# Performance work log

Hardware: AMD Instinct MI355X
Metric: run time of the kernel (lower is better)

Reference implementation:

```python
import jax, jax.numpy as jnp
import numpy as np

DIM = 192  # init dim; input channels = 2*DIM, output channels = DIM
EPS = 1e-5


def setup_inputs() -> dict:
    key = jax.random.key(0)
    k1, k2 = jax.random.split(key)
    x = jax.random.normal(k1, (2, 16, 32, 32, 2 * DIM), dtype=jnp.float32)
    W = jax.random.normal(k2, (2 * DIM, 8 * DIM), dtype=jnp.float32) * 0.02
    gamma = jnp.ones((2 * DIM,), dtype=jnp.float32)
    beta = jnp.zeros((2 * DIM,), dtype=jnp.float32)
    return {"x": x, "W": W, "gamma": gamma, "beta": beta}


def reference(x, W, gamma, beta):
    dim = DIM
    b, d, h, w, c = x.shape  # c == 2*dim
    # LayerNorm over last dim (biased variance, as torch)
    mu = jnp.mean(x, axis=-1, keepdims=True)
    var = jnp.var(x, axis=-1, keepdims=True)
    xn = (x - mu) * jax.lax.rsqrt(var + EPS) * gamma + beta
    # Linear expansion 2*dim -> 8*dim (no bias)
    xe = jnp.einsum('bdhwc,ce->bdhwe', xn, W)  # (b,d,h,w,8*dim)
    ch = lambda i: xe[..., i * dim:(i + 1) * dim]
    z = jnp.zeros((b, d, h, w, dim), dtype=xe.dtype)
    # Faithful to the torch code: parities (0,1,0) and (0,0,1) are written
    # are NEVER written (stay zero). Index = pd*4 + ph*2 + pw.
    grid = jnp.stack([
        ch(0), ch(6),  # (0,0,0), (0,0,1)
        ch(5), z,      # (0,1,0), (0,1,1)
        ch(1), ch(4),  # (1,0,0), (1,0,1)
        z,     ch(7),  # (1,1,0), (1,1,1)
    ], axis=4)  # (b,d,h,w,8,dim)
    grid = grid.reshape(b, d, h, w, 2, 2, 2, dim)
    # interleave parity axes: (b, d,pd, h,ph, w,pw, dim) -> (b,2d,2h,2w,dim)
    out = grid.transpose(0, 1, 4, 2, 5, 3, 6, 7).reshape(b, 2 * d, 2 * h, 2 * w, dim)
    return out
```

## Files before the change

### kernel.cpp

```cpp
#include <hip/hip_runtime.h>
#include <hip/hip_bf16.h>
#include <stdint.h>


typedef __attribute__((ext_vector_type(4))) float f32x4;
typedef __attribute__((ext_vector_type(8))) short s16x8;
typedef __attribute__((ext_vector_type(4))) unsigned short u16x4;
typedef const __attribute__((address_space(1))) void gvoid_t;
typedef __attribute__((address_space(3))) void lvoid_t;

__device__ __forceinline__ int ob_of_p(int p) {
    const int w = p & 31, h = (p >> 5) & 31, d = (p >> 10) & 15, b = p >> 14;
    return b * 25165824 + d * 1572864 + h * 24576 + w * 384;
}

__device__ __forceinline__ unsigned short f2bf(float f) {
    unsigned u = __builtin_bit_cast(unsigned, f);
    u += 0x7fffu + ((u >> 16) & 1u);
    return (unsigned short)(u >> 16);
}

__global__ __launch_bounds__(256) void ln_kernel(const float* __restrict__ x,
                                                 const float* __restrict__ gamma,
                                                 const float* __restrict__ beta,
                                                 float* __restrict__ outf) {
    const int wv = threadIdx.x >> 6;
    const int l  = threadIdx.x & 63;
    const int p  = blockIdx.x * 4 + wv;
    const float* row = x + (size_t)p * 384;
    f32x4 v0 = *(const f32x4*)(row + l * 4);
    f32x4 v1 = {0.f, 0.f, 0.f, 0.f};
    if (l < 32) v1 = *(const f32x4*)(row + 256 + l * 4);
    float s  = v0[0]+v0[1]+v0[2]+v0[3] + v1[0]+v1[1]+v1[2]+v1[3];
    float s2 = v0[0]*v0[0]+v0[1]*v0[1]+v0[2]*v0[2]+v0[3]*v0[3]
             + v1[0]*v1[0]+v1[1]*v1[1]+v1[2]*v1[2]+v1[3]*v1[3];
    #pragma unroll
    for (int off = 32; off >= 1; off >>= 1) {
        s  += __shfl_xor(s,  off);
        s2 += __shfl_xor(s2, off);
    }
    const float mu = s * (1.f / 384.f);
    const float rs = rsqrtf(s2 * (1.f / 384.f) - mu * mu + 1e-5f);
    unsigned short* dst = (unsigned short*)(outf + ob_of_p(p) + 12480);
    f32x4 g0 = *(const f32x4*)(gamma + l * 4);
    f32x4 b0 = *(const f32x4*)(beta  + l * 4);
    u16x4 o0;
    #pragma unroll
    for (int j = 0; j < 4; ++j) o0[j] = f2bf((v0[j] - mu) * rs * g0[j] + b0[j]);
    *(u16x4*)(dst + l * 4) = o0;
    if (l < 32) {
        f32x4 g1 = *(const f32x4*)(gamma + 256 + l * 4);
        f32x4 b1 = *(const f32x4*)(beta  + 256 + l * 4);
        u16x4 o1;
        #pragma unroll
        for (int j = 0; j < 4; ++j) o1[j] = f2bf((v1[j] - mu) * rs * g1[j] + b1[j]);
        *(u16x4*)(dst + 256 + l * 4) = o1;
    }
}

__global__ __launch_bounds__(256) void wt_kernel(const float* __restrict__ W,
                                                 float* __restrict__ outf) {
    const int t = blockIdx.x * 256 + threadIdx.x;
    const int k = t % 384;
    const int n = t / 384;
    const int s = n / 192;
    const int oc = (s < 2 ? s : s + 2) * 192 + (n % 192);
    const float v = W[(size_t)k * 1536 + oc];
    unsigned short* dst = (unsigned short*)(outf + ob_of_p(n) + 798720);
    dst[k] = f2bf(v);
}

__global__ __launch_bounds__(256) void gemm_kernel(float* __restrict__ outf) {
    __shared__ char lds[32768];
    const char* gbase = (const char*)outf;
    const int tid = threadIdx.x;
    const int wv = tid >> 6, l = tid & 63;
    int bid = blockIdx.x;
    bid = (bid & 7) * 288 + (bid >> 3);
    const int mt = bid / 9, nt = bid % 9;
    const int m0 = mt * 128, n0 = nt * 128;

    size_t srcA[4], srcB[4];
    int ldsA[4], ldsB[4];
    #pragma unroll
    for (int i = 0; i < 4; ++i) {
        const int r = wv * 32 + i * 8 + (l >> 3);
        const int swz = ((l & 7) * 16) ^ ((r & 7) << 4);
        srcA[i] = (size_t)(ob_of_p(m0 + r) + 12480)  * 4 + swz;
        srcB[i] = (size_t)(ob_of_p(n0 + r) + 798720) * 4 + swz;
        ldsA[i] = (wv * 32 + i * 8) * 128;
        ldsB[i] = 16384 + (wv * 32 + i * 8) * 128;
    }

    f32x4 acc[4][4];
    const f32x4 fz = {0.f, 0.f, 0.f, 0.f};
    #pragma unroll
    for (int m = 0; m < 4; ++m)
        #pragma unroll
        for (int n = 0; n < 4; ++n) acc[m][n] = fz;

    const int wm = wv >> 1, wn = wv & 1;
    int arow[4], brow[4];
    #pragma unroll
    for (int i = 0; i < 4; ++i) {
        arow[i] = wm * 64 + i * 16 + (l & 15);
        brow[i] = wn * 64 + i * 16 + (l & 15);
    }
    const int kbyte0 = (l >> 4) * 16;

    for (int t = 0; t < 6; ++t) {
        const int kb = t * 128;
        #pragma unroll
        for (int i = 0; i < 4; ++i)
            __builtin_amdgcn_global_load_lds((gvoid_t*)(gbase + srcA[i] + kb),
                                             (lvoid_t*)(lds + ldsA[i]), 16, 0, 0);
        #pragma unroll
        for (int i = 0; i < 4; ++i)
            __builtin_amdgcn_global_load_lds((gvoid_t*)(gbase + srcB[i] + kb),
                                             (lvoid_t*)(lds + ldsB[i]), 16, 0, 0);
        __syncthreads();
        #pragma unroll
        for (int kk = 0; kk < 2; ++kk) {
            const int kbyte = kbyte0 + kk * 64;
            s16x8 a[4], b[4];
            #pragma unroll
            for (int m = 0; m < 4; ++m)
                a[m] = *(const s16x8*)(lds + arow[m] * 128 + (kbyte ^ ((arow[m] & 7) << 4)));
            #pragma unroll
            for (int n = 0; n < 4; ++n)
                b[n] = *(const s16x8*)(lds + 16384 + brow[n] * 128 + (kbyte ^ ((brow[n] & 7) << 4)));
            #pragma unroll
            for (int m = 0; m < 4; ++m)
                #pragma unroll
                for (int n = 0; n < 4; ++n)
                    acc[m][n] = __builtin_amdgcn_mfma_f32_16x16x32_bf16(a[m], b[n], acc[m][n], 0, 0, 0);
        }
        __syncthreads();
    }

    int coladd[4];
    #pragma unroll
    for (int n = 0; n < 4; ++n) {
        const int gnb = n0 + wn * 64 + n * 16;
        const int s = gnb / 192;
        int d;
        if      (s == 0) d = 0;
        else if (s == 1) d = 786432;
        else if (s == 2) d = 786624;
        else if (s == 3) d = 12288;
        else if (s == 4) d = 192;
        else             d = 798912;
        coladd[n] = d + (gnb % 192) + (l & 15);
    }
    const int pb = m0 + wm * 64 + (l >> 4) * 4;
    #pragma unroll
    for (int m = 0; m < 4; ++m) {
        #pragma unroll
        for (int r = 0; r < 4; ++r) {
            const int p  = pb + m * 16 + r;
            const int ob = ob_of_p(p);
            #pragma unroll
            for (int n = 0; n < 4; ++n)
                outf[ob + coladd[n]] = acc[m][n][r];
        }
    }
}

__global__ __launch_bounds__(256) void zero_kernel(float* __restrict__ outf) {
    const int idx = blockIdx.x * 256 + threadIdx.x;
    const int f4 = idx % 48;
    const int pr = (idx / 48) & 1;
    const int p  = idx / 96;
    const f32x4 z = {0.f, 0.f, 0.f, 0.f};
    *(f32x4*)(outf + ob_of_p(p) + (pr ? 798720 : 12480) + f4 * 4) = z;
}

extern "C" void kernel_launch(void* const* d_in, const int* in_sizes, int n_in,
                              void* d_out, int out_size, void* d_ws, size_t ws_size,
                              hipStream_t stream) {
    const float* x     = (const float*)d_in[0];
    const float* W     = (const float*)d_in[1];
    const float* gamma = (const float*)d_in[2];
    const float* beta  = (const float*)d_in[3];
    float* out = (float*)d_out;
    ln_kernel  <<<8192,  256, 0, stream>>>(x, gamma, beta, out);
    wt_kernel  <<<1728,  256, 0, stream>>>(W, out);
    gemm_kernel<<<2304,  256, 0, stream>>>(out);
    zero_kernel<<<12288, 256, 0, stream>>>(out);
}
```

Measured before the change: 86.04 us.

## Stage operands in workspace, fuse zero fill into LN, double-buffer GEMM A tiles

When the workspace is large enough, the normalized activations and the reordered bf16 weights go to a contiguous workspace buffer instead of being scattered into the zero slots of the output. The zero-slot fill moves into the LayerNorm kernel, which removes the separate zero kernel launch. The GEMM reads B fragments straight from global memory into registers and double-buffers the A tile in LDS, overlapping the next tile's load with the MFMAs using explicit vmcnt waits. The cost is extra workspace memory and more fragile hand-written scheduling and waitcnt logic. The old path is kept as a fallback when the workspace is too small.

```diff
diff --git a/kernel.cpp b/kernel.cpp
--- a/kernel.cpp
+++ b/kernel.cpp
@@ -19,6 +19,169 @@
     u += 0x7fffu + ((u >> 16) & 1u);
     return (unsigned short)(u >> 16);
 }
+
+
+__global__ __launch_bounds__(256) void ln2_kernel(const float* __restrict__ x,
+                                                  const float* __restrict__ gamma,
+                                                  const float* __restrict__ beta,
+                                                  float* __restrict__ outf,
+                                                  unsigned short* __restrict__ xn) {
+    const int wv = threadIdx.x >> 6;
+    const int l  = threadIdx.x & 63;
+    const int p  = blockIdx.x * 4 + wv;
+    const float* row = x + (size_t)p * 384;
+    f32x4 v0 = *(const f32x4*)(row + l * 4);
+    f32x4 v1 = {0.f, 0.f, 0.f, 0.f};
+    if (l < 32) v1 = *(const f32x4*)(row + 256 + l * 4);
+    float s  = v0[0]+v0[1]+v0[2]+v0[3] + v1[0]+v1[1]+v1[2]+v1[3];
+    float s2 = v0[0]*v0[0]+v0[1]*v0[1]+v0[2]*v0[2]+v0[3]*v0[3]
+             + v1[0]*v1[0]+v1[1]*v1[1]+v1[2]*v1[2]+v1[3]*v1[3];
+    #pragma unroll
+    for (int off = 32; off >= 1; off >>= 1) {
+        s  += __shfl_xor(s,  off);
+        s2 += __shfl_xor(s2, off);
+    }
+    const float mu = s * (1.f / 384.f);
+    const float rs = rsqrtf(s2 * (1.f / 384.f) - mu * mu + 1e-5f);
+    unsigned short* dst = xn + (size_t)p * 384;
+    f32x4 g0 = *(const f32x4*)(gamma + l * 4);
+    f32x4 b0 = *(const f32x4*)(beta  + l * 4);
+    u16x4 o0;
+    #pragma unroll
+    for (int j = 0; j < 4; ++j) o0[j] = f2bf((v0[j] - mu) * rs * g0[j] + b0[j]);
+    *(u16x4*)(dst + l * 4) = o0;
+    if (l < 32) {
+        f32x4 g1 = *(const f32x4*)(gamma + 256 + l * 4);
+        f32x4 b1 = *(const f32x4*)(beta  + 256 + l * 4);
+        u16x4 o1;
+        #pragma unroll
+        for (int j = 0; j < 4; ++j) o1[j] = f2bf((v1[j] - mu) * rs * g1[j] + b1[j]);
+        *(u16x4*)(dst + 256 + l * 4) = o1;
+    }
+    if (l < 48) {
+        const int ob = ob_of_p(p);
+        const f32x4 z = {0.f, 0.f, 0.f, 0.f};
+        *(f32x4*)(outf + ob + 12480  + l * 4) = z;
+        *(f32x4*)(outf + ob + 798720 + l * 4) = z;
+    }
+}
+
+__global__ __launch_bounds__(256) void wt2_kernel(const float* __restrict__ W,
+                                                  unsigned short* __restrict__ wt) {
+    const int t = blockIdx.x * 256 + threadIdx.x;
+    const int k = t % 384;
+    const int n = t / 384;
+    const int s = n / 192;
+    const int oc = (s < 2 ? s : s + 2) * 192 + (n % 192);
+    wt[(size_t)n * 384 + k] = f2bf(W[(size_t)k * 1536 + oc]);
+}
+
+__global__ __launch_bounds__(256) void gemm2_kernel(const unsigned short* __restrict__ xn,
+                                                    const unsigned short* __restrict__ wt,
+                                                    float* __restrict__ outf) {
+    __shared__ char lds[32768];
+    const char* xb = (const char*)xn;
+    const char* wb = (const char*)wt;
+    const int tid = threadIdx.x;
+    const int wv = tid >> 6, l = tid & 63;
+    int bid = blockIdx.x;
+    bid = (bid & 7) * 288 + (bid >> 3);
+    const int mt = bid / 9, nt = bid % 9;
+    const int m0 = mt * 128, n0 = nt * 128;
+    const int wm = wv >> 1, wn = wv & 1;
+
+    size_t srcA[4]; int ldsA[4];
+    #pragma unroll
+    for (int i = 0; i < 4; ++i) {
+        const int r = wv * 32 + i * 8 + (l >> 3);
+        srcA[i] = (size_t)(m0 + r) * 768 + (((l & 7) * 16) ^ ((r & 7) << 4));
+        ldsA[i] = (wv * 32 + i * 8) * 128;
+    }
+    const char* bsrc = wb + (size_t)(n0 + wn * 64 + (l & 15)) * 768 + (l >> 4) * 16;
+
+    int arow[4];
+    #pragma unroll
+    for (int m = 0; m < 4; ++m) arow[m] = wm * 64 + m * 16 + (l & 15);
+    const int kb0 = (l >> 4) * 16;
+
+    f32x4 acc[4][4];
+    const f32x4 fz = {0.f, 0.f, 0.f, 0.f};
+    #pragma unroll
+    for (int m = 0; m < 4; ++m)
+        #pragma unroll
+        for (int n = 0; n < 4; ++n) acc[m][n] = fz;
+
+    #pragma unroll
+    for (int i = 0; i < 4; ++i)
+        __builtin_amdgcn_global_load_lds((gvoid_t*)(xb + srcA[i]),
+                                         (lvoid_t*)(lds + ldsA[i]), 16, 0, 0);
+
+    #pragma unroll
+    for (int t = 0; t < 6; ++t) {
+        const int cur = (t & 1) * 16384, nxt = cur ^ 16384;
+        s16x8 b[4][2];
+        #pragma unroll
+        for (int n = 0; n < 4; ++n)
+            #pragma unroll
+            for (int kk = 0; kk < 2; ++kk)
+                b[n][kk] = *(const s16x8*)(bsrc + n * 12288 + t * 128 + kk * 64);
+        __builtin_amdgcn_sched_barrier(0);
+        if (t < 5) {
+            #pragma unroll
+            for (int i = 0; i < 4; ++i)
+                __builtin_amdgcn_global_load_lds((gvoid_t*)(xb + srcA[i] + (t + 1) * 128),
+                                                 (lvoid_t*)(lds + nxt + ldsA[i]), 16, 0, 0);
+        }
+        __builtin_amdgcn_sched_barrier(0);
+        if (t < 5) asm volatile("s_waitcnt vmcnt(12)");
+        else       asm volatile("s_waitcnt vmcnt(8)");
+        __builtin_amdgcn_sched_barrier(0);
+        __builtin_amdgcn_s_barrier();
+        __builtin_amdgcn_sched_barrier(0);
+        #pragma unroll
+        for (int kk = 0; kk < 2; ++kk) {
+            s16x8 a[4];
+            #pragma unroll
+            for (int m = 0; m < 4; ++m)
+                a[m] = *(const s16x8*)(lds + cur + arow[m] * 128 +
+                                       ((kb0 + kk * 64) ^ ((arow[m] & 7) << 4)));
+            #pragma unroll
+            for (int m = 0; m < 4; ++m)
+                #pragma unroll
+                for (int n = 0; n < 4; ++n)
+                    acc[m][n] = __builtin_amdgcn_mfma_f32_16x16x32_bf16(a[m], b[n][kk], acc[m][n], 0, 0, 0);
+        }
+        __builtin_amdgcn_s_barrier();
+        __builtin_amdgcn_sched_barrier(0);
+    }
+
+    int coladd[4];
+    #pragma unroll
+    for (int n = 0; n < 4; ++n) {
+        const int gnb = n0 + wn * 64 + n * 16;
+        const int s = gnb / 192;
+        int d;
+        if      (s == 0) d = 0;
+        else if (s == 1) d = 786432;
+        else if (s == 2) d = 786624;
+        else if (s == 3) d = 12288;
+        else if (s == 4) d = 192;
+        else             d = 798912;
+        coladd[n] = d + (gnb % 192) + (l & 15);
+    }
+    const int pb = m0 + wm * 64 + (l >> 4) * 4;
+    #pragma unroll
+    for (int m = 0; m < 4; ++m) {
+        #pragma unroll
+        for (int r = 0; r < 4; ++r) {
+            const int ob = ob_of_p(pb + m * 16 + r);
+            #pragma unroll
+            for (int n = 0; n < 4; ++n)
+                outf[ob + coladd[n]] = acc[m][n][r];
+        }
+    }
+}
+
 
 __global__ __launch_bounds__(256) void ln_kernel(const float* __restrict__ x,
                                                  const float* __restrict__ gamma,
@@ -79,7 +242,6 @@
     bid = (bid & 7) * 288 + (bid >> 3);
     const int mt = bid / 9, nt = bid % 9;
     const int m0 = mt * 128, n0 = nt * 128;
-
     size_t srcA[4], srcB[4];
     int ldsA[4], ldsB[4];
     #pragma unroll
@@ -91,14 +253,12 @@
         ldsA[i] = (wv * 32 + i * 8) * 128;
         ldsB[i] = 16384 + (wv * 32 + i * 8) * 128;
     }
-
     f32x4 acc[4][4];
     const f32x4 fz = {0.f, 0.f, 0.f, 0.f};
     #pragma unroll
     for (int m = 0; m < 4; ++m)
         #pragma unroll
         for (int n = 0; n < 4; ++n) acc[m][n] = fz;
-
     const int wm = wv >> 1, wn = wv & 1;
     int arow[4], brow[4];
     #pragma unroll
@@ -107,7 +267,6 @@
         brow[i] = wn * 64 + i * 16 + (l & 15);
     }
     const int kbyte0 = (l >> 4) * 16;
-
     for (int t = 0; t < 6; ++t) {
         const int kb = t * 128;
         #pragma unroll
@@ -137,7 +296,6 @@
         }
         __syncthreads();
     }
-
     int coladd[4];
     #pragma unroll
     for (int n = 0; n < 4; ++n) {
@@ -157,8 +315,7 @@
     for (int m = 0; m < 4; ++m) {
         #pragma unroll
         for (int r = 0; r < 4; ++r) {
-            const int p  = pb + m * 16 + r;
-            const int ob = ob_of_p(p);
+            const int ob = ob_of_p(pb + m * 16 + r);
             #pragma unroll
             for (int n = 0; n < 4; ++n)
                 outf[ob + coladd[n]] = acc[m][n][r];
@@ -174,6 +331,7 @@
     const f32x4 z = {0.f, 0.f, 0.f, 0.f};
     *(f32x4*)(outf + ob_of_p(p) + (pr ? 798720 : 12480) + f4 * 4) = z;
 }
+
 
 extern "C" void kernel_launch(void* const* d_in, const int* in_sizes, int n_in,
                               void* d_out, int out_size, void* d_ws, size_t ws_size,
@@ -183,8 +341,17 @@
     const float* gamma = (const float*)d_in[2];
     const float* beta  = (const float*)d_in[3];
     float* out = (float*)d_out;
-    ln_kernel  <<<8192,  256, 0, stream>>>(x, gamma, beta, out);
-    wt_kernel  <<<1728,  256, 0, stream>>>(W, out);
-    gemm_kernel<<<2304,  256, 0, stream>>>(out);
-    zero_kernel<<<12288, 256, 0, stream>>>(out);
-}
+    const size_t need = 25165824 + 884736;
+    if (ws_size >= need) {
+        unsigned short* xn = (unsigned short*)d_ws;
+        unsigned short* wt = (unsigned short*)((char*)d_ws + 25165824);
+        ln2_kernel  <<<8192, 256, 0, stream>>>(x, gamma, beta, out, xn);
+        wt2_kernel  <<<1728, 256, 0, stream>>>(W, wt);
+        gemm2_kernel<<<2304, 256, 0, stream>>>(xn, wt, out);
+    } else {
+        ln_kernel  <<<8192,  256, 0, stream>>>(x, gamma, beta, out);
+        wt_kernel  <<<1728,  256, 0, stream>>>(W, out);
+        gemm_kernel<<<2304,  256, 0, stream>>>(out);
+        zero_kernel<<<12288, 256, 0, stream>>>(out);
+    }
+}
```

Result: slower. 99.49 us (+15.6%).
